# Performance work log

Measured on AMD Instinct MI355X. Metric: run time of the kernel, lower is better.

The kernel has to match this reference:

```python
import jax, jax.numpy as jnp
import numpy as np

T, B, D, H = 512, 64, 512, 512  # seq_len, batch, input_size, hidden_size


def setup_inputs() -> dict:
    key = jax.random.key(0)
    ks = jax.random.split(key, 7)
    s = 1.0 / np.sqrt(H)
    return {
        "input": jax.random.normal(ks[0], (T, B, D), dtype=jnp.float32),
        "h0": jax.random.normal(ks[1], (B, H), dtype=jnp.float32),
        "c0": jax.random.normal(ks[2], (B, H), dtype=jnp.float32),
        "W_ih": jax.random.normal(ks[3], (4 * H, D), dtype=jnp.float32) * s,
        "W_hh": jax.random.normal(ks[4], (4 * H, H), dtype=jnp.float32) * s,
        "b_ih": jax.random.normal(ks[5], (4 * H,), dtype=jnp.float32) * s,
        "b_hh": jax.random.normal(ks[6], (4 * H,), dtype=jnp.float32) * s,
        "batch_first": 0,
    }


def reference(input, h0, c0, W_ih, W_hh, b_ih, b_hh, batch_first):
    # Dense (non-packed) branch of RNNLayer.forward with an LSTM cell.
    x = jnp.swapaxes(input, 0, 1) if batch_first else input  # [T, B, D]
    # Input projection is independent of the recurrence: precompute for all t.
    x_proj = jnp.einsum('tbd,gd->tbg', x, W_ih) + b_ih  # [T, B, 4H]

    def step(carry, xt):
        h, c = carry
        gates = xt + h @ W_hh.T + b_hh  # [B, 4H]
        i, f, g, o = jnp.split(gates, 4, axis=-1)
        c_new = jax.nn.sigmoid(f) * c + jax.nn.sigmoid(i) * jnp.tanh(g)
        h_new = jax.nn.sigmoid(o) * jnp.tanh(c_new)
        return (h_new, c_new), h_new

    (hT, cT), ys = jax.lax.scan(step, (h0, c0), x_proj)  # ys: [T, B, H]
    outputs = jnp.swapaxes(ys, 0, 1) if batch_first else ys
    return outputs, hT, cT
```

## Files before the change

kernel.cpp:

```cpp
#include <hip/hip_runtime.h>

typedef __attribute__((ext_vector_type(8))) short bfrag;
typedef __attribute__((ext_vector_type(4))) float f32x4;
typedef __attribute__((ext_vector_type(4))) int i32x4;

#define NT 512
#define NB 64
#define KD 512
#define NG 2048
#define GB 4
#define GH 16

#define YS_SZ (NT * NB * KD)
#define HT_OFF YS_SZ
#define CT_OFF (YS_SZ + NB * KD)

#define MB_BLK_WORDS 4096
#define MB_PAR_WORDS (GB * MB_BLK_WORDS)
#define MB_BYTES (2 * MB_PAR_WORDS * 8)

__device__ __forceinline__ unsigned short f2bf(float f) {
  unsigned u = __float_as_uint(f);
  u += 0x7fffu + ((u >> 16) & 1u);
  return (unsigned short)(u >> 16);
}
__device__ __forceinline__ float bf2f(unsigned short h) {
  return __uint_as_float(((unsigned)h) << 16);
}
__device__ __forceinline__ float sigm(float v) { return 1.f / (1.f + __expf(-v)); }
__device__ __forceinline__ float tanh_f(float v) { return 1.f - 2.f / (__expf(2.f * v) + 1.f); }

__global__ __launch_bounds__(256) void cvt_bf16(const float* __restrict__ src,
                                                unsigned short* __restrict__ dst, int n8) {
  int i = blockIdx.x * 256 + threadIdx.x;
  if (i >= n8) return;
  const float4 a = *(const float4*)(src + (size_t)i * 8);
  const float4 b = *(const float4*)(src + (size_t)i * 8 + 4);
  i32x4 v;
  v.x = (int)(f2bf(a.x) | ((unsigned)f2bf(a.y) << 16));
  v.y = (int)(f2bf(a.z) | ((unsigned)f2bf(a.w) << 16));
  v.z = (int)(f2bf(b.x) | ((unsigned)f2bf(b.y) << 16));
  v.w = (int)(f2bf(b.z) | ((unsigned)f2bf(b.w) << 16));
  *(i32x4*)(dst + (size_t)i * 8) = v;
}

template <int XP32>
__global__ __launch_bounds__(256) void xproj_gemm(const unsigned short* __restrict__ Wb,
                                                  const unsigned short* __restrict__ Xb,
                                                  const float* __restrict__ bias,
                                                  void* __restrict__ XPv) {
  __shared__ unsigned short Wt[64 * 40];
  __shared__ unsigned short Xt[64 * 40];
  const int tid = threadIdx.x;
  const int lane = tid & 63, wid = tid >> 6;
  const int g = lane >> 4, cc = lane & 15;
  const int n0 = blockIdx.x * 64;
  const int t = blockIdx.y;
  const size_t m0 = (size_t)t * 64;
  const int srow = tid >> 2, schunk = (tid & 3) * 8;

  f32x4 acc[4] = {};
  for (int kb = 0; kb < KD; kb += 32) {
    __syncthreads();
    *(i32x4*)&Wt[srow * 40 + schunk] = *(const i32x4*)(Wb + (size_t)(n0 + srow) * KD + kb + schunk);
    *(i32x4*)&Xt[srow * 40 + schunk] = *(const i32x4*)(Xb + (m0 + srow) * KD + kb + schunk);
    __syncthreads();
    bfrag af = *(const bfrag*)&Wt[(wid * 16 + cc) * 40 + g * 8];
#pragma unroll
    for (int mt = 0; mt < 4; ++mt) {
      bfrag bf = *(const bfrag*)&Xt[(mt * 16 + cc) * 40 + g * 8];
      acc[mt] = __builtin_amdgcn_mfma_f32_16x16x32_bf16(af, bf, acc[mt], 0, 0, 0);
    }
  }
  const int nl = wid * 16 + g * 4;
  float bi[4];
#pragma unroll
  for (int r = 0; r < 4; ++r) bi[r] = bias[n0 + nl + r];
#pragma unroll
  for (int mt = 0; mt < 4; ++mt) {
#pragma unroll
    for (int r = 0; r < 4; ++r) {
      float v = acc[mt][r] + bi[r];
      size_t idx = ((size_t)t * NG + n0 + nl + r) * 64 + mt * 16 + cc;
      if (XP32) ((float*)XPv)[idx] = v;
      else ((unsigned short*)XPv)[idx] = f2bf(v);
    }
  }
}

template <int XP32>
__global__ __launch_bounds__(256, 1) void lstm_rec(const unsigned short* __restrict__ Whh,
                                                   const void* __restrict__ XPv,
                                                   const float* __restrict__ bhh,
                                                   const float* __restrict__ h0,
                                                   const float* __restrict__ c0,
                                                   unsigned long long* __restrict__ mbox,
                                                   float* __restrict__ out) {
  __shared__ unsigned short hl[16 * 512];
  __shared__ float hf[16 * 33];

  const int tid = threadIdx.x;
  const int lane = tid & 63, wid = tid >> 6;
  const int g = lane >> 4, cc = lane & 15;
  const int blk = blockIdx.x >> 4, slice = blockIdx.x & 15;
  const int b0 = blk * 16, d0 = slice * 32;

  {
    const int lp = tid >> 4, b = tid & 15;
    const int d = d0 + lp * 2;
    const float* hp = h0 + (size_t)(b0 + b) * KD + d;
    unsigned d32 = (unsigned)f2bf(hp[0]) | ((unsigned)f2bf(hp[1]) << 16);
    __hip_atomic_store(mbox + (size_t)blk * MB_BLK_WORDS + ((d0 >> 1) + lp) * 16 + b,
                       (1ull << 32) | (unsigned long long)d32, __ATOMIC_RELAXED,
                       __HIP_MEMORY_SCOPE_AGENT);
  }

  bfrag w[2][16];
#pragma unroll
  for (int j = 0; j < 2; ++j) {
    const int tt = wid * 2 + j;
    const int r = tt * 16 + cc;
    const size_t n = (size_t)(r & 3) * KD + d0 + (r >> 2);
#pragma unroll
    for (int ks = 0; ks < 16; ++ks)
      w[j][ks] = *(const bfrag*)(Whh + n * KD + ks * 32 + g * 8);
  }
  float bh[2][4], creg[2];
#pragma unroll
  for (int j = 0; j < 2; ++j) {
    const int d = d0 + (wid * 2 + j) * 4 + g;
#pragma unroll
    for (int r = 0; r < 4; ++r) bh[j][r] = bhh[r * KD + d];
    creg[j] = c0[(b0 + cc) * KD + d];
  }

  for (int t = 0; t < NT; ++t) {
    float xp[2][4];
#pragma unroll
    for (int j = 0; j < 2; ++j) {
      const int d = d0 + (wid * 2 + j) * 4 + g;
#pragma unroll
      for (int r = 0; r < 4; ++r) {
        size_t idx = ((size_t)t * NG + r * KD + d) * 64 + b0 + cc;
        xp[j][r] = XP32 ? ((const float*)XPv)[idx] : bf2f(((const unsigned short*)XPv)[idx]);
      }
    }
    const unsigned long long* mbr =
        mbox + (size_t)(t & 1) * MB_PAR_WORDS + (size_t)blk * MB_BLK_WORDS;
    const unsigned tg = (unsigned)(t + 1);
    unsigned long long q0, q1, q2, q3, q4, q5, q6, q7, q8, q9, q10, q11, q12, q13, q14, q15;
#define PISSUE(r)                                                        \
  asm volatile("global_load_dwordx2 %0, %1, %2 sc1"                      \
               : "=v"(q##r)                                              \
               : "v"((unsigned)(tid * 8 + r * 2048)), "s"(mbr));
    for (;;) {
      PISSUE(0) PISSUE(1) PISSUE(2) PISSUE(3) PISSUE(4) PISSUE(5) PISSUE(6) PISSUE(7)
      PISSUE(8) PISSUE(9) PISSUE(10) PISSUE(11) PISSUE(12) PISSUE(13) PISSUE(14) PISSUE(15)
      asm volatile("s_waitcnt vmcnt(0)" ::: "memory");
      __builtin_amdgcn_sched_barrier(0);
      unsigned ok = 1u;
#define PCHK(r) ok &= ((unsigned)(q##r >> 32) == tg) ? 1u : 0u;
      PCHK(0) PCHK(1) PCHK(2) PCHK(3) PCHK(4) PCHK(5) PCHK(6) PCHK(7)
      PCHK(8) PCHK(9) PCHK(10) PCHK(11) PCHK(12) PCHK(13) PCHK(14) PCHK(15)
      if (__all(ok)) break;
    }
#undef PISSUE
#undef PCHK
    {
      const int b = tid & 15, pq = tid >> 4;
      const int bb = b * 1024, bx = (b & 7) << 4;
#define PUNP(r) \
  *(unsigned*)((char*)hl + bb + (((r * 16 + pq) * 4) ^ bx)) = (unsigned)q##r;
      PUNP(0) PUNP(1) PUNP(2) PUNP(3) PUNP(4) PUNP(5) PUNP(6) PUNP(7)
      PUNP(8) PUNP(9) PUNP(10) PUNP(11) PUNP(12) PUNP(13) PUNP(14) PUNP(15)
#undef PUNP
    }
    __syncthreads();
    f32x4 p00 = {0.f, 0.f, 0.f, 0.f}, p01 = {0.f, 0.f, 0.f, 0.f};
    f32x4 p10 = {0.f, 0.f, 0.f, 0.f}, p11 = {0.f, 0.f, 0.f, 0.f};
#pragma unroll
    for (int ks = 0; ks < 8; ++ks) {
      const int off = ks * 64 + g * 16;
      bfrag hb = *(const bfrag*)((const char*)hl + cc * 1024 + (off ^ ((cc & 7) << 4)));
      p00 = __builtin_amdgcn_mfma_f32_16x16x32_bf16(w[0][ks], hb, p00, 0, 0, 0);
      p10 = __builtin_amdgcn_mfma_f32_16x16x32_bf16(w[1][ks], hb, p10, 0, 0, 0);
    }
#pragma unroll
    for (int ks = 8; ks < 16; ++ks) {
      const int off = ks * 64 + g * 16;
      bfrag hb = *(const bfrag*)((const char*)hl + cc * 1024 + (off ^ ((cc & 7) << 4)));
      p01 = __builtin_amdgcn_mfma_f32_16x16x32_bf16(w[0][ks], hb, p01, 0, 0, 0);
      p11 = __builtin_amdgcn_mfma_f32_16x16x32_bf16(w[1][ks], hb, p11, 0, 0, 0);
    }
    const f32x4 acc0 = p00 + p01, acc1 = p10 + p11;
    float hnv[2];
#pragma unroll
    for (int j = 0; j < 2; ++j) {
      const f32x4 a = j ? acc1 : acc0;
      float gi = a[0] + xp[j][0] + bh[j][0];
      float gf = a[1] + xp[j][1] + bh[j][1];
      float gg = a[2] + xp[j][2] + bh[j][2];
      float go = a[3] + xp[j][3] + bh[j][3];
      float cn = sigm(gf) * creg[j] + sigm(gi) * tanh_f(gg);
      creg[j] = cn;
      hnv[j] = sigm(go) * tanh_f(cn);
      if (t == NT - 1) out[CT_OFF + (size_t)(b0 + cc) * KD + d0 + (wid * 8 + j * 4 + g)] = cn;
    }
    {
      unsigned long long* mbw =
          mbox + (size_t)((t + 1) & 1) * MB_PAR_WORDS + (size_t)blk * MB_BLK_WORDS;
      const unsigned long long tagn = (unsigned long long)(unsigned)(t + 2) << 32;
      const float o0 = __shfl_xor(hnv[0], 16);
      const float o1 = __shfl_xor(hnv[1], 16);
      if (!(g & 1)) {
        const unsigned w0 = (unsigned)f2bf(hnv[0]) | ((unsigned)f2bf(o0) << 16);
        const unsigned w1 = (unsigned)f2bf(hnv[1]) | ((unsigned)f2bf(o1) << 16);
        const int p0 = (d0 >> 1) + wid * 4 + (g >> 1);
        const int p1 = p0 + 2;
        __hip_atomic_store(mbw + p0 * 16 + cc, tagn | (unsigned long long)w0,
                           __ATOMIC_RELAXED, __HIP_MEMORY_SCOPE_AGENT);
        __hip_atomic_store(mbw + p1 * 16 + cc, tagn | (unsigned long long)w1,
                           __ATOMIC_RELAXED, __HIP_MEMORY_SCOPE_AGENT);
      }
    }
#pragma unroll
    for (int j = 0; j < 2; ++j) hf[cc * 33 + (wid * 8 + j * 4 + g)] = hnv[j];
    __syncthreads();
    if (tid < 128) {
      const int b = tid >> 3, dg = (tid & 7) * 4;
      float4 hv;
      hv.x = hf[b * 33 + dg];
      hv.y = hf[b * 33 + dg + 1];
      hv.z = hf[b * 33 + dg + 2];
      hv.w = hf[b * 33 + dg + 3];
      *(float4*)(out + (size_t)t * NB * KD + (size_t)(b0 + b) * KD + d0 + dg) = hv;
      if (t == NT - 1)
        *(float4*)(out + HT_OFF + (size_t)(b0 + b) * KD + d0 + dg) = hv;
    }
  }
}

extern "C" void kernel_launch(void* const* d_in, const int* in_sizes, int n_in,
                              void* d_out, int out_size, void* d_ws, size_t ws_size,
                              hipStream_t stream) {
  const float* x = (const float*)d_in[0];
  const float* h0 = (const float*)d_in[1];
  const float* c0 = (const float*)d_in[2];
  const float* Wih = (const float*)d_in[3];
  const float* Whh = (const float*)d_in[4];
  const float* bih = (const float*)d_in[5];
  const float* bhh = (const float*)d_in[6];
  float* out = (float*)d_out;
  char* ws = (char*)d_ws;

  unsigned long long* mbox = (unsigned long long*)ws;
  unsigned short* WhhB = (unsigned short*)(ws + MB_BYTES);
  unsigned short* WihB = (unsigned short*)(ws + MB_BYTES + 2097152);
  unsigned short* XB = (unsigned short*)(ws + MB_BYTES + 2 * 2097152);
  const size_t xp_off = MB_BYTES + 2ull * 2097152 + 33554432;
  void* XP = (void*)(ws + xp_off);
  const bool xp32 = ws_size >= xp_off + (size_t)NT * NG * 64 * 4;

  hipMemsetAsync(ws, 0, MB_BYTES, stream);

  const int nx8 = NT * NB * KD / 8;
  const int nw8 = NG * KD / 8;
  cvt_bf16<<<dim3(nx8 / 256), 256, 0, stream>>>(x, XB, nx8);
  cvt_bf16<<<dim3(nw8 / 256), 256, 0, stream>>>(Wih, WihB, nw8);
  cvt_bf16<<<dim3(nw8 / 256), 256, 0, stream>>>(Whh, WhhB, nw8);

  if (xp32) {
    xproj_gemm<1><<<dim3(NG / 64, NT), 256, 0, stream>>>(WihB, XB, bih, XP);
    lstm_rec<1><<<dim3(GB * GH), 256, 0, stream>>>(WhhB, XP, bhh, h0, c0, mbox, out);
  } else {
    xproj_gemm<0><<<dim3(NG / 64, NT), 256, 0, stream>>>(WihB, XB, bih, XP);
    lstm_rec<0><<<dim3(GB * GH), 256, 0, stream>>>(WhhB, XP, bhh, h0, c0, mbox, out);
  }
}
```

Before: 1.461 ms.

## Prefetch mailbox and x_proj loads early; drop shared-memory output staging and barrier

The tagged mailbox loads for the next step are issued speculatively at the end of the current step. The x_proj loads for a step are issued as raw asm before waiting on the mailbox, so both overlap with other work; the re-poll loop now runs only when the tags are stale. The shared-memory transpose of h into float4 stores, and its second __syncthreads per step, is replaced by direct scalar stores from each lane. This shortens the serial critical path of each recurrent step. The cost is less coalesced output writes, and correctness now relies on hand-counted vmcnt waits and on the implicit cross-wave ordering that the mailbox provides.

```diff
diff --git a/kernel.cpp b/kernel.cpp
--- a/kernel.cpp
+++ b/kernel.cpp
@@ -97,7 +97,6 @@
                                                    unsigned long long* __restrict__ mbox,
                                                    float* __restrict__ out) {
   __shared__ unsigned short hl[16 * 512];
-  __shared__ float hf[16 * 33];
 
   const int tid = threadIdx.x;
   const int lane = tid & 63, wid = tid >> 6;
@@ -134,38 +133,67 @@
     creg[j] = c0[(b0 + cc) * KD + d];
   }
 
+  unsigned long long q0, q1, q2, q3, q4, q5, q6, q7, q8, q9, q10, q11, q12, q13, q14, q15;
+
+#define PISSUE(MB, r)                                                       \
+  asm volatile("global_load_dwordx2 %0, %1, %2 sc1"                         \
+               : "=v"(q##r)                                                 \
+               : "v"((unsigned)(tid * 8 + r * 2048)), "s"(MB) : "memory")
+#define PISSUE_ALL(MB)                                                      \
+  do {                                                                      \
+    PISSUE(MB, 0); PISSUE(MB, 1); PISSUE(MB, 2); PISSUE(MB, 3);             \
+    PISSUE(MB, 4); PISSUE(MB, 5); PISSUE(MB, 6); PISSUE(MB, 7);             \
+    PISSUE(MB, 8); PISSUE(MB, 9); PISSUE(MB, 10); PISSUE(MB, 11);           \
+    PISSUE(MB, 12); PISSUE(MB, 13); PISSUE(MB, 14); PISSUE(MB, 15);         \
+  } while (0)
+#define PCHK_ALL(okv, tg)                                                   \
+  do {                                                                      \
+    okv = 1u;                                                               \
+    okv &= ((unsigned)(q0 >> 32) == (tg)); okv &= ((unsigned)(q1 >> 32) == (tg));   \
+    okv &= ((unsigned)(q2 >> 32) == (tg)); okv &= ((unsigned)(q3 >> 32) == (tg));   \
+    okv &= ((unsigned)(q4 >> 32) == (tg)); okv &= ((unsigned)(q5 >> 32) == (tg));   \
+    okv &= ((unsigned)(q6 >> 32) == (tg)); okv &= ((unsigned)(q7 >> 32) == (tg));   \
+    okv &= ((unsigned)(q8 >> 32) == (tg)); okv &= ((unsigned)(q9 >> 32) == (tg));   \
+    okv &= ((unsigned)(q10 >> 32) == (tg)); okv &= ((unsigned)(q11 >> 32) == (tg)); \
+    okv &= ((unsigned)(q12 >> 32) == (tg)); okv &= ((unsigned)(q13 >> 32) == (tg)); \
+    okv &= ((unsigned)(q14 >> 32) == (tg)); okv &= ((unsigned)(q15 >> 32) == (tg)); \
+  } while (0)
+
+  {
+    const unsigned long long* nb = mbox + (size_t)blk * MB_BLK_WORDS;
+    PISSUE_ALL(nb);
+  }
+
   for (int t = 0; t < NT; ++t) {
-    float xp[2][4];
+    unsigned xpr[2][4];
 #pragma unroll
     for (int j = 0; j < 2; ++j) {
       const int d = d0 + (wid * 2 + j) * 4 + g;
 #pragma unroll
       for (int r = 0; r < 4; ++r) {
-        size_t idx = ((size_t)t * NG + r * KD + d) * 64 + b0 + cc;
-        xp[j][r] = XP32 ? ((const float*)XPv)[idx] : bf2f(((const unsigned short*)XPv)[idx]);
+        const size_t idx = ((size_t)t * NG + r * KD + d) * 64 + b0 + cc;
+        if constexpr (XP32) {
+          const float* p = (const float*)XPv + idx;
+          asm volatile("global_load_dword %0, %1, off" : "=v"(xpr[j][r]) : "v"(p) : "memory");
+        } else {
+          const unsigned short* p = (const unsigned short*)XPv + idx;
+          asm volatile("global_load_ushort %0, %1, off" : "=v"(xpr[j][r]) : "v"(p) : "memory");
+        }
       }
     }
     const unsigned long long* mbr =
         mbox + (size_t)(t & 1) * MB_PAR_WORDS + (size_t)blk * MB_BLK_WORDS;
     const unsigned tg = (unsigned)(t + 1);
-    unsigned long long q0, q1, q2, q3, q4, q5, q6, q7, q8, q9, q10, q11, q12, q13, q14, q15;
-#define PISSUE(r)                                                        \
-  asm volatile("global_load_dwordx2 %0, %1, %2 sc1"                      \
-               : "=v"(q##r)                                              \
-               : "v"((unsigned)(tid * 8 + r * 2048)), "s"(mbr));
-    for (;;) {
-      PISSUE(0) PISSUE(1) PISSUE(2) PISSUE(3) PISSUE(4) PISSUE(5) PISSUE(6) PISSUE(7)
-      PISSUE(8) PISSUE(9) PISSUE(10) PISSUE(11) PISSUE(12) PISSUE(13) PISSUE(14) PISSUE(15)
+    asm volatile("s_waitcnt vmcnt(8)" ::: "memory");
+    __builtin_amdgcn_sched_barrier(0);
+    unsigned ok;
+    PCHK_ALL(ok, tg);
+    while (!__all(ok)) {
+      PISSUE_ALL(mbr);
       asm volatile("s_waitcnt vmcnt(0)" ::: "memory");
       __builtin_amdgcn_sched_barrier(0);
-      unsigned ok = 1u;
-#define PCHK(r) ok &= ((unsigned)(q##r >> 32) == tg) ? 1u : 0u;
-      PCHK(0) PCHK(1) PCHK(2) PCHK(3) PCHK(4) PCHK(5) PCHK(6) PCHK(7)
-      PCHK(8) PCHK(9) PCHK(10) PCHK(11) PCHK(12) PCHK(13) PCHK(14) PCHK(15)
-      if (__all(ok)) break;
-    }
-#undef PISSUE
-#undef PCHK
+      PCHK_ALL(ok, tg);
+    }
     {
       const int b = tid & 15, pq = tid >> 4;
       const int bb = b * 1024, bx = (b & 7) << 4;
@@ -193,18 +221,27 @@
       p11 = __builtin_amdgcn_mfma_f32_16x16x32_bf16(w[1][ks], hb, p11, 0, 0, 0);
     }
     const f32x4 acc0 = p00 + p01, acc1 = p10 + p11;
+    asm volatile("s_waitcnt vmcnt(0)" ::: "memory");
+    __builtin_amdgcn_sched_barrier(0);
     float hnv[2];
 #pragma unroll
     for (int j = 0; j < 2; ++j) {
       const f32x4 a = j ? acc1 : acc0;
-      float gi = a[0] + xp[j][0] + bh[j][0];
-      float gf = a[1] + xp[j][1] + bh[j][1];
-      float gg = a[2] + xp[j][2] + bh[j][2];
-      float go = a[3] + xp[j][3] + bh[j][3];
+      float x0, x1, x2, x3;
+      if constexpr (XP32) {
+        x0 = __uint_as_float(xpr[j][0]); x1 = __uint_as_float(xpr[j][1]);
+        x2 = __uint_as_float(xpr[j][2]); x3 = __uint_as_float(xpr[j][3]);
+      } else {
+        x0 = bf2f((unsigned short)xpr[j][0]); x1 = bf2f((unsigned short)xpr[j][1]);
+        x2 = bf2f((unsigned short)xpr[j][2]); x3 = bf2f((unsigned short)xpr[j][3]);
+      }
+      float gi = a[0] + x0 + bh[j][0];
+      float gf = a[1] + x1 + bh[j][1];
+      float gg = a[2] + x2 + bh[j][2];
+      float go = a[3] + x3 + bh[j][3];
       float cn = sigm(gf) * creg[j] + sigm(gi) * tanh_f(gg);
       creg[j] = cn;
       hnv[j] = sigm(go) * tanh_f(cn);
-      if (t == NT - 1) out[CT_OFF + (size_t)(b0 + cc) * KD + d0 + (wid * 8 + j * 4 + g)] = cn;
     }
     {
       unsigned long long* mbw =
@@ -223,21 +260,28 @@
                            __ATOMIC_RELAXED, __HIP_MEMORY_SCOPE_AGENT);
       }
     }
-#pragma unroll
-    for (int j = 0; j < 2; ++j) hf[cc * 33 + (wid * 8 + j * 4 + g)] = hnv[j];
-    __syncthreads();
-    if (tid < 128) {
-      const int b = tid >> 3, dg = (tid & 7) * 4;
-      float4 hv;
-      hv.x = hf[b * 33 + dg];
-      hv.y = hf[b * 33 + dg + 1];
-      hv.z = hf[b * 33 + dg + 2];
-      hv.w = hf[b * 33 + dg + 3];
-      *(float4*)(out + (size_t)t * NB * KD + (size_t)(b0 + b) * KD + d0 + dg) = hv;
-      if (t == NT - 1)
-        *(float4*)(out + HT_OFF + (size_t)(b0 + b) * KD + d0 + dg) = hv;
-    }
-  }
+    {
+      float* yb = out + (size_t)t * NB * KD + (size_t)(b0 + cc) * KD + d0 + wid * 8 + g;
+      yb[0] = hnv[0];
+      yb[4] = hnv[1];
+      if (t == NT - 1) {
+        float* hb = out + HT_OFF + (size_t)(b0 + cc) * KD + d0 + wid * 8 + g;
+        hb[0] = hnv[0];
+        hb[4] = hnv[1];
+        float* cb = out + CT_OFF + (size_t)(b0 + cc) * KD + d0 + wid * 8 + g;
+        cb[0] = creg[0];
+        cb[4] = creg[1];
+      }
+    }
+    {
+      const unsigned long long* nb =
+          mbox + (size_t)((t + 1) & 1) * MB_PAR_WORDS + (size_t)blk * MB_BLK_WORDS;
+      PISSUE_ALL(nb);
+    }
+  }
+#undef PISSUE
+#undef PISSUE_ALL
+#undef PCHK_ALL
 }
 
 extern "C" void kernel_launch(void* const* d_in, const int* in_sizes, int n_in,
```

Result: no change. 1.486 ms (+1.7%).

## Fuse input projection into persistent LSTM kernel with producer-consumer overlap

Applied to the files above, without the earlier changes.

Merges the input-projection GEMM and the recurrent kernel into one persistent launch. 64 blocks run the recurrence while 192 worker blocks compute per-timestep projection tiles and signal completion through per-timestep atomic counters. The recurrent blocks poll these counters, and the check for the next step is folded into the existing mailbox poll. The separate x and W_hh bf16 conversion kernels are dropped in favour of converting inline. The aim is to hide the GEMM behind the sequential recurrence and remove extra launches and passes over memory, at the risk that worker blocks compete with the recurrent blocks for bandwidth and that co-residency of all 256 blocks is required.

```diff
diff --git a/kernel.cpp b/kernel.cpp
--- a/kernel.cpp
+++ b/kernel.cpp
@@ -10,6 +10,10 @@
 #define NG 2048
 #define GB 4
 #define GH 16
+#define NWREC 64
+#define NWGF 256
+#define NWORK (NWGF - NWREC)
+#define NJOBS (32 * NT)
 
 #define YS_SZ (NT * NB * KD)
 #define HT_OFF YS_SZ
@@ -45,63 +49,79 @@
 }
 
 template <int XP32>
-__global__ __launch_bounds__(256) void xproj_gemm(const unsigned short* __restrict__ Wb,
-                                                  const unsigned short* __restrict__ Xb,
-                                                  const float* __restrict__ bias,
-                                                  void* __restrict__ XPv) {
+__global__ __launch_bounds__(256, 1) void lstm_fused(const float* __restrict__ Whh,
+                                                     const unsigned short* __restrict__ WihB,
+                                                     const float* __restrict__ x,
+                                                     void* __restrict__ XPv,
+                                                     const float* __restrict__ bih,
+                                                     const float* __restrict__ bhh,
+                                                     const float* __restrict__ h0,
+                                                     const float* __restrict__ c0,
+                                                     unsigned long long* __restrict__ mbox,
+                                                     unsigned int* __restrict__ xcnt,
+                                                     float* __restrict__ out) {
+  __shared__ unsigned short hl[16 * 512];
+  __shared__ float hf[16 * 33];
   __shared__ unsigned short Wt[64 * 40];
   __shared__ unsigned short Xt[64 * 40];
+
   const int tid = threadIdx.x;
   const int lane = tid & 63, wid = tid >> 6;
   const int g = lane >> 4, cc = lane & 15;
-  const int n0 = blockIdx.x * 64;
-  const int t = blockIdx.y;
-  const size_t m0 = (size_t)t * 64;
-  const int srow = tid >> 2, schunk = (tid & 3) * 8;
-
-  f32x4 acc[4] = {};
-  for (int kb = 0; kb < KD; kb += 32) {
-    __syncthreads();
-    *(i32x4*)&Wt[srow * 40 + schunk] = *(const i32x4*)(Wb + (size_t)(n0 + srow) * KD + kb + schunk);
-    *(i32x4*)&Xt[srow * 40 + schunk] = *(const i32x4*)(Xb + (m0 + srow) * KD + kb + schunk);
-    __syncthreads();
-    bfrag af = *(const bfrag*)&Wt[(wid * 16 + cc) * 40 + g * 8];
-#pragma unroll
-    for (int mt = 0; mt < 4; ++mt) {
-      bfrag bf = *(const bfrag*)&Xt[(mt * 16 + cc) * 40 + g * 8];
-      acc[mt] = __builtin_amdgcn_mfma_f32_16x16x32_bf16(af, bf, acc[mt], 0, 0, 0);
-    }
-  }
-  const int nl = wid * 16 + g * 4;
-  float bi[4];
-#pragma unroll
-  for (int r = 0; r < 4; ++r) bi[r] = bias[n0 + nl + r];
-#pragma unroll
-  for (int mt = 0; mt < 4; ++mt) {
-#pragma unroll
-    for (int r = 0; r < 4; ++r) {
-      float v = acc[mt][r] + bi[r];
-      size_t idx = ((size_t)t * NG + n0 + nl + r) * 64 + mt * 16 + cc;
-      if (XP32) ((float*)XPv)[idx] = v;
-      else ((unsigned short*)XPv)[idx] = f2bf(v);
-    }
-  }
-}
-
-template <int XP32>
-__global__ __launch_bounds__(256, 1) void lstm_rec(const unsigned short* __restrict__ Whh,
-                                                   const void* __restrict__ XPv,
-                                                   const float* __restrict__ bhh,
-                                                   const float* __restrict__ h0,
-                                                   const float* __restrict__ c0,
-                                                   unsigned long long* __restrict__ mbox,
-                                                   float* __restrict__ out) {
-  __shared__ unsigned short hl[16 * 512];
-  __shared__ float hf[16 * 33];
-
-  const int tid = threadIdx.x;
-  const int lane = tid & 63, wid = tid >> 6;
-  const int g = lane >> 4, cc = lane & 15;
+
+  if (blockIdx.x >= NWREC) {
+    const int srow = tid >> 2, schunk = (tid & 3) * 8;
+    for (int jj = (int)blockIdx.x - NWREC; jj < NJOBS; jj += NWORK) {
+      const int t = jj >> 5, n0 = (jj & 31) << 6;
+      f32x4 acc[4] = {};
+      for (int kb = 0; kb < KD; kb += 32) {
+        __syncthreads();
+        *(i32x4*)&Wt[srow * 40 + schunk] =
+            *(const i32x4*)(WihB + (size_t)(n0 + srow) * KD + kb + schunk);
+        {
+          const float* xs = x + ((size_t)t * 64 + srow) * KD + kb + schunk;
+          const float4 a = *(const float4*)xs;
+          const float4 b = *(const float4*)(xs + 4);
+          i32x4 v;
+          v.x = (int)(f2bf(a.x) | ((unsigned)f2bf(a.y) << 16));
+          v.y = (int)(f2bf(a.z) | ((unsigned)f2bf(a.w) << 16));
+          v.z = (int)(f2bf(b.x) | ((unsigned)f2bf(b.y) << 16));
+          v.w = (int)(f2bf(b.z) | ((unsigned)f2bf(b.w) << 16));
+          *(i32x4*)&Xt[srow * 40 + schunk] = v;
+        }
+        __syncthreads();
+        bfrag af = *(const bfrag*)&Wt[(wid * 16 + cc) * 40 + g * 8];
+#pragma unroll
+        for (int mt = 0; mt < 4; ++mt) {
+          bfrag bf = *(const bfrag*)&Xt[(mt * 16 + cc) * 40 + g * 8];
+          acc[mt] = __builtin_amdgcn_mfma_f32_16x16x32_bf16(af, bf, acc[mt], 0, 0, 0);
+        }
+      }
+      const int nl = wid * 16 + g * 4;
+      float bi[4];
+#pragma unroll
+      for (int r = 0; r < 4; ++r) bi[r] = bih[n0 + nl + r];
+#pragma unroll
+      for (int mt = 0; mt < 4; ++mt) {
+#pragma unroll
+        for (int r = 0; r < 4; ++r) {
+          float v = acc[mt][r] + bi[r];
+          size_t idx = ((size_t)t * NG + n0 + nl + r) * 64 + mt * 16 + cc;
+          if constexpr (XP32)
+            __hip_atomic_store((unsigned*)XPv + idx, __float_as_uint(v), __ATOMIC_RELAXED,
+                               __HIP_MEMORY_SCOPE_AGENT);
+          else
+            __hip_atomic_store((unsigned short*)XPv + idx, f2bf(v), __ATOMIC_RELAXED,
+                               __HIP_MEMORY_SCOPE_AGENT);
+        }
+      }
+      __syncthreads();
+      if (tid == 0)
+        __hip_atomic_fetch_add(xcnt + t, 1u, __ATOMIC_RELAXED, __HIP_MEMORY_SCOPE_AGENT);
+    }
+    return;
+  }
+
   const int blk = blockIdx.x >> 4, slice = blockIdx.x & 15;
   const int b0 = blk * 16, d0 = slice * 32;
 
@@ -122,8 +142,17 @@
     const int r = tt * 16 + cc;
     const size_t n = (size_t)(r & 3) * KD + d0 + (r >> 2);
 #pragma unroll
-    for (int ks = 0; ks < 16; ++ks)
-      w[j][ks] = *(const bfrag*)(Whh + n * KD + ks * 32 + g * 8);
+    for (int ks = 0; ks < 16; ++ks) {
+      const float* wp = Whh + n * KD + ks * 32 + g * 8;
+      const float4 a = *(const float4*)wp;
+      const float4 b = *(const float4*)(wp + 4);
+      bfrag fr;
+      fr[0] = (short)f2bf(a.x); fr[1] = (short)f2bf(a.y);
+      fr[2] = (short)f2bf(a.z); fr[3] = (short)f2bf(a.w);
+      fr[4] = (short)f2bf(b.x); fr[5] = (short)f2bf(b.y);
+      fr[6] = (short)f2bf(b.z); fr[7] = (short)f2bf(b.w);
+      w[j][ks] = fr;
+    }
   }
   float bh[2][4], creg[2];
 #pragma unroll
@@ -134,7 +163,18 @@
     creg[j] = c0[(b0 + cc) * KD + d];
   }
 
+  bool cnt_ok = false;
+
   for (int t = 0; t < NT; ++t) {
+    if (!cnt_ok) {
+      const unsigned int* cp = xcnt + t;
+      for (;;) {
+        unsigned c;
+        asm volatile("global_load_dword %0, %1, off sc1\n\ts_waitcnt vmcnt(0)"
+                     : "=&v"(c) : "v"(cp) : "memory");
+        if (__all(c >= 32u)) break;
+      }
+    }
     float xp[2][4];
 #pragma unroll
     for (int j = 0; j < 2; ++j) {
@@ -142,12 +182,22 @@
 #pragma unroll
       for (int r = 0; r < 4; ++r) {
         size_t idx = ((size_t)t * NG + r * KD + d) * 64 + b0 + cc;
-        xp[j][r] = XP32 ? ((const float*)XPv)[idx] : bf2f(((const unsigned short*)XPv)[idx]);
+        if constexpr (XP32) {
+          unsigned uv = __hip_atomic_load((const unsigned*)XPv + idx, __ATOMIC_RELAXED,
+                                          __HIP_MEMORY_SCOPE_AGENT);
+          xp[j][r] = __uint_as_float(uv);
+        } else {
+          unsigned short sv = __hip_atomic_load((const unsigned short*)XPv + idx,
+                                                __ATOMIC_RELAXED, __HIP_MEMORY_SCOPE_AGENT);
+          xp[j][r] = bf2f(sv);
+        }
       }
     }
     const unsigned long long* mbr =
         mbox + (size_t)(t & 1) * MB_PAR_WORDS + (size_t)blk * MB_BLK_WORDS;
+    const unsigned int* cpn = xcnt + t + 1;
     const unsigned tg = (unsigned)(t + 1);
+    unsigned cn;
     unsigned long long q0, q1, q2, q3, q4, q5, q6, q7, q8, q9, q10, q11, q12, q13, q14, q15;
 #define PISSUE(r)                                                        \
   asm volatile("global_load_dwordx2 %0, %1, %2 sc1"                      \
@@ -156,6 +206,7 @@
     for (;;) {
       PISSUE(0) PISSUE(1) PISSUE(2) PISSUE(3) PISSUE(4) PISSUE(5) PISSUE(6) PISSUE(7)
       PISSUE(8) PISSUE(9) PISSUE(10) PISSUE(11) PISSUE(12) PISSUE(13) PISSUE(14) PISSUE(15)
+      asm volatile("global_load_dword %0, %1, off sc1" : "=v"(cn) : "v"(cpn));
       asm volatile("s_waitcnt vmcnt(0)" ::: "memory");
       __builtin_amdgcn_sched_barrier(0);
       unsigned ok = 1u;
@@ -166,6 +217,7 @@
     }
 #undef PISSUE
 #undef PCHK
+    cnt_ok = __all(cn >= 32u);
     {
       const int b = tid & 15, pq = tid >> 4;
       const int bb = b * 1024, bx = (b & 7) << 4;
@@ -201,10 +253,10 @@
       float gf = a[1] + xp[j][1] + bh[j][1];
       float gg = a[2] + xp[j][2] + bh[j][2];
       float go = a[3] + xp[j][3] + bh[j][3];
-      float cn = sigm(gf) * creg[j] + sigm(gi) * tanh_f(gg);
-      creg[j] = cn;
-      hnv[j] = sigm(go) * tanh_f(cn);
-      if (t == NT - 1) out[CT_OFF + (size_t)(b0 + cc) * KD + d0 + (wid * 8 + j * 4 + g)] = cn;
+      float cn2 = sigm(gf) * creg[j] + sigm(gi) * tanh_f(gg);
+      creg[j] = cn2;
+      hnv[j] = sigm(go) * tanh_f(cn2);
+      if (t == NT - 1) out[CT_OFF + (size_t)(b0 + cc) * KD + d0 + (wid * 8 + j * 4 + g)] = cn2;
     }
     {
       unsigned long long* mbw =
@@ -254,26 +306,22 @@
   char* ws = (char*)d_ws;
 
   unsigned long long* mbox = (unsigned long long*)ws;
-  unsigned short* WhhB = (unsigned short*)(ws + MB_BYTES);
-  unsigned short* WihB = (unsigned short*)(ws + MB_BYTES + 2097152);
-  unsigned short* XB = (unsigned short*)(ws + MB_BYTES + 2 * 2097152);
-  const size_t xp_off = MB_BYTES + 2ull * 2097152 + 33554432;
+  unsigned int* xcnt = (unsigned int*)(ws + MB_BYTES);
+  unsigned short* WihB = (unsigned short*)(ws + MB_BYTES + 4096);
+  const size_t xp_off = MB_BYTES + 4096 + 2097152;
   void* XP = (void*)(ws + xp_off);
   const bool xp32 = ws_size >= xp_off + (size_t)NT * NG * 64 * 4;
 
-  hipMemsetAsync(ws, 0, MB_BYTES, stream);
-
-  const int nx8 = NT * NB * KD / 8;
+  hipMemsetAsync(ws, 0, MB_BYTES + 4096, stream);
+
   const int nw8 = NG * KD / 8;
-  cvt_bf16<<<dim3(nx8 / 256), 256, 0, stream>>>(x, XB, nx8);
   cvt_bf16<<<dim3(nw8 / 256), 256, 0, stream>>>(Wih, WihB, nw8);
-  cvt_bf16<<<dim3(nw8 / 256), 256, 0, stream>>>(Whh, WhhB, nw8);
 
   if (xp32) {
-    xproj_gemm<1><<<dim3(NG / 64, NT), 256, 0, stream>>>(WihB, XB, bih, XP);
-    lstm_rec<1><<<dim3(GB * GH), 256, 0, stream>>>(WhhB, XP, bhh, h0, c0, mbox, out);
+    lstm_fused<1><<<dim3(NWGF), 256, 0, stream>>>(Whh, WihB, x, XP, bih, bhh, h0, c0,
+                                                  mbox, xcnt, out);
   } else {
-    xproj_gemm<0><<<dim3(NG / 64, NT), 256, 0, stream>>>(WihB, XB, bih, XP);
-    lstm_rec<0><<<dim3(GB * GH), 256, 0, stream>>>(WhhB, XP, bhh, h0, c0, mbox, out);
-  }
-}
+    lstm_fused<0><<<dim3(NWGF), 256, 0, stream>>>(Whh, WihB, x, XP, bih, bhh, h0, c0,
+                                                  mbox, xcnt, out);
+  }
+}
```

Measured after the change: 1.510 ms. 3.3% more time.
